# Kernel tuning notes

Measured on AMD Instinct MI355X. Metric: run time of the kernel, lower is better.

## Reference

```python
import jax, jax.numpy as jnp
import numpy as np

B, F, H = 32768, 128, 64  # batch, input_size, hidden width (n_layers=(64,64))


def setup_inputs() -> dict:
    key = jax.random.key(0)
    ks = jax.random.split(key, 8)
    s1 = 1.0  # fan_in=1 for first layer
    sH = 1.0 / np.sqrt(H)
    return {
        "x": jax.random.normal(ks[0], (B, F), dtype=jnp.float32),
        "w1": jax.random.uniform(ks[1], (F, H), jnp.float32, -s1, s1),
        "b1": jax.random.uniform(ks[2], (F, H), jnp.float32, -s1, s1),
        "w2": jax.random.uniform(ks[3], (F, H, H), jnp.float32, -sH, sH),
        "b2": jax.random.uniform(ks[4], (F, H), jnp.float32, -sH, sH),
        "w3": jax.random.uniform(ks[5], (F, H), jnp.float32, -sH, sH),
        "b3": jax.random.uniform(ks[6], (F,), jnp.float32, -sH, sH),
        "bias": jnp.zeros((1,), dtype=jnp.float32),
    }


def reference(x, w1, b1, w2, b2, w3, b3, bias):
    # Per-feature tiny MLP, batched over all F features at once.
    # Layer 1: Linear(1 -> H): h1[b,f,h] = x[b,f]*w1[f,h] + b1[f,h]
    h1 = jax.nn.relu(x[:, :, None] * w1[None] + b1[None])        # (B, F, H)
    # Layer 2: Linear(H -> H) per feature (grouped GEMM)
    h2 = jax.nn.relu(jnp.einsum("bfh,fhg->bfg", h1, w2) + b2[None])  # (B, F, H)
    # Output layer: Linear(H -> 1) per feature -> contribution (B, F)
    contrib = jnp.einsum("bfh,fh->bf", h2, w3) + b3[None]        # (B, F)
    logit = contrib.sum(axis=-1) + bias                          # (B,)
    p = jax.nn.sigmoid(logit)
    return jnp.stack([1.0 - p, p], axis=1)                       # (B, 2)
```

## Files before the change

kernel.cpp:

```cpp
#include <hip/hip_runtime.h>
#include <hip/hip_bf16.h>
#include <hip/hip_fp16.h>


#define B_SZ 32768
#define F_SZ 128
#define H_SZ 64

typedef _Float16 half8 __attribute__((ext_vector_type(8)));
typedef float floatx4 __attribute__((ext_vector_type(4)));

union U8 { half8 v; unsigned u[4]; };

__device__ __forceinline__ unsigned pkh(float lo, float hi) {
    __half2 h = __float22half2_rn(make_float2(lo, hi));
    return __builtin_bit_cast(unsigned, h);
}

__device__ __forceinline__ unsigned cpk(float lo, float hi) {
    return __builtin_bit_cast(unsigned, __builtin_amdgcn_cvt_pkrtz(lo, hi));
}

__device__ __forceinline__ unsigned relu2(unsigned a) {
    unsigned r;
    asm("v_pk_max_f16 %0, %1, %2" : "=v"(r) : "v"(a), "v"(0u));
    return r;
}

__device__ __forceinline__ float fdot2(unsigned a, unsigned b, float c) {
    float d;
    asm("v_dot2_f32_f16 %0, %1, %2, %3" : "=v"(d) : "v"(a), "v"(b), "v"(c));
    return d;
}

__device__ __forceinline__ __half2 bch2(unsigned u) {
    return __builtin_bit_cast(__half2, u);
}

__global__ __launch_bounds__(256, 3)
void nam_main(const float* __restrict__ x,
              const float* __restrict__ w1, const float* __restrict__ b1,
              const float* __restrict__ b2, const float* __restrict__ w3,
              const float* __restrict__ b3,
              const float* __restrict__ w2,
              float* __restrict__ part)
{
    __shared__ float partial[4][512];

    const int tid  = threadIdx.x;
    const int lane = tid & 63;
    const int wv   = tid >> 6;
    const int l15  = lane & 15;
    const int quad = lane >> 4;
    const int rg   = blockIdx.x & 63;
    const int gf   = blockIdx.x >> 6;
    const int f    = gf * 4 + wv;
    const int rb   = rg * 512;

    const float* w2f = w2 + (size_t)f * H_SZ * H_SZ;
    half8 wfrag[4][2];
    #pragma unroll
    for (int gt = 0; gt < 4; ++gt)
        #pragma unroll
        for (int ks = 0; ks < 2; ++ks) {
            const float* src = w2f + (ks * 32 + quad * 8) * H_SZ + gt * 16 + l15;
            U8 o;
            #pragma unroll
            for (int t = 0; t < 4; ++t)
                o.u[t] = pkh(src[(2 * t) * H_SZ], src[(2 * t + 1) * H_SZ]);
            wfrag[gt][ks] = o.v;
        }

    unsigned wk2[2][4], bk2[2][4];
    #pragma unroll
    for (int ks = 0; ks < 2; ++ks) {
        float wtmp[8], btmp[8];
        const float4* wq = (const float4*)(w1 + f * 64 + ks * 32 + quad * 8);
        const float4* bq = (const float4*)(b1 + f * 64 + ks * 32 + quad * 8);
        *(float4*)&wtmp[0] = wq[0]; *(float4*)&wtmp[4] = wq[1];
        *(float4*)&btmp[0] = bq[0]; *(float4*)&btmp[4] = bq[1];
        #pragma unroll
        for (int t = 0; t < 4; ++t) {
            wk2[ks][t] = pkh(wtmp[2 * t], wtmp[2 * t + 1]);
            bk2[ks][t] = pkh(btmp[2 * t], btmp[2 * t + 1]);
        }
    }

    floatx4 b2c[4];
    unsigned w3h[4][2];
    #pragma unroll
    for (int gt = 0; gt < 4; ++gt) {
        float4 bv  = *(const float4*)(b2 + f * 64 + gt * 16 + quad * 4);
        float4 wv3 = *(const float4*)(w3 + f * 64 + gt * 16 + quad * 4);
        b2c[gt] = floatx4{bv.x, bv.y, bv.z, bv.w};
        w3h[gt][0] = pkh(wv3.x, wv3.y);
        w3h[gt][1] = pkh(wv3.z, wv3.w);
    }
    const float b3f = b3[f];

    float xv = x[(size_t)(rb + lane) * F_SZ + f];

    #pragma unroll 1
    for (int c = 0; c < 8; ++c) {
        float xvn;
        if (c < 7)
            xvn = x[(size_t)(rb + (c + 1) * 64 + lane) * F_SZ + f];

        unsigned xpk = __builtin_bit_cast(unsigned, __float2half2_rn(xv));
        unsigned xf[4];
        #pragma unroll
        for (int bt = 0; bt < 4; ++bt)
            xf[bt] = (unsigned)__shfl((int)xpk, bt * 16 + l15, 64);

        half8 hfrag[4][2];
        #pragma unroll
        for (int ks = 0; ks < 2; ++ks)
            #pragma unroll
            for (int bt = 0; bt < 4; ++bt) {
                U8 o;
                #pragma unroll
                for (int t = 0; t < 4; ++t) {
                    __half2 h = __hfma2(bch2(xf[bt]), bch2(wk2[ks][t]), bch2(bk2[ks][t]));
                    o.u[t] = relu2(__builtin_bit_cast(unsigned, h));
                }
                hfrag[bt][ks] = o.v;
            }

        float ta[4] = {0.0f, 0.0f, 0.0f, 0.0f};
        float tb[4] = {0.0f, 0.0f, 0.0f, 0.0f};
        __builtin_amdgcn_s_setprio(1);
        #pragma unroll
        for (int gt = 0; gt < 4; ++gt)
            #pragma unroll
            for (int bt = 0; bt < 4; ++bt) {
                floatx4 acc = __builtin_amdgcn_mfma_f32_16x16x32_f16(
                    wfrag[gt][0], hfrag[bt][0], b2c[gt], 0, 0, 0);
                acc = __builtin_amdgcn_mfma_f32_16x16x32_f16(
                    wfrag[gt][1], hfrag[bt][1], acc, 0, 0, 0);
                unsigned p0 = relu2(cpk(acc[0], acc[1]));
                unsigned p1 = relu2(cpk(acc[2], acc[3]));
                ta[bt] = fdot2(p0, w3h[gt][0], ta[bt]);
                tb[bt] = fdot2(p1, w3h[gt][1], tb[bt]);
            }
        __builtin_amdgcn_s_setprio(0);

        float t[4];
        #pragma unroll
        for (int bt = 0; bt < 4; ++bt) {
            t[bt] = ta[bt] + tb[bt];
            t[bt] += __shfl_xor(t[bt], 16, 64);
            t[bt] += __shfl_xor(t[bt], 32, 64);
        }
        if (quad == 0) {
            #pragma unroll
            for (int bt = 0; bt < 4; ++bt)
                partial[wv][c * 64 + bt * 16 + l15] = t[bt] + b3f;
        }

        xv = xvn;
    }

    __syncthreads();

    #pragma unroll
    for (int k = 0; k < 2; ++k) {
        int row = k * 256 + tid;
        float p = partial[0][row] + partial[1][row]
                + partial[2][row] + partial[3][row];
        part[(size_t)gf * B_SZ + rb + row] = p;
    }
}

__global__ __launch_bounds__(256)
void nam_final(const float* __restrict__ part, const float* __restrict__ bias,
               float* __restrict__ out)
{
    int b = blockIdx.x * 256 + threadIdx.x;
    float s = bias[0];
    #pragma unroll
    for (int gf = 0; gf < 32; ++gf)
        s += part[(size_t)gf * B_SZ + b];
    float p = 1.0f / (1.0f + __expf(-s));
    ((float2*)out)[b] = make_float2(1.0f - p, p);
}

extern "C" void kernel_launch(void* const* d_in, const int* in_sizes, int n_in,
                              void* d_out, int out_size, void* d_ws, size_t ws_size,
                              hipStream_t stream)
{
    const float* x    = (const float*)d_in[0];
    const float* w1   = (const float*)d_in[1];
    const float* b1   = (const float*)d_in[2];
    const float* w2   = (const float*)d_in[3];
    const float* b2   = (const float*)d_in[4];
    const float* w3   = (const float*)d_in[5];
    const float* b3   = (const float*)d_in[6];
    const float* bias = (const float*)d_in[7];
    float* out = (float*)d_out;

    float* part = (float*)d_ws;

    nam_main<<<dim3(2048), dim3(256), 0, stream>>>(
        x, w1, b1, b2, w3, b3, w2, part);
    nam_final<<<dim3(B_SZ / 256), dim3(256), 0, stream>>>(part, bias, out);
}
```

Baseline: 115.9 us.

## Fuse final reduction into main kernel via atomics and last-block sigmoid

```diff
diff --git a/kernel.cpp b/kernel.cpp
--- a/kernel.cpp
+++ b/kernel.cpp
@@ -43,9 +43,13 @@
               const float* __restrict__ b2, const float* __restrict__ w3,
               const float* __restrict__ b3,
               const float* __restrict__ w2,
-              float* __restrict__ part)
+              const float* __restrict__ bias,
+              float* __restrict__ logitacc,
+              unsigned* __restrict__ cnt,
+              float* __restrict__ out)
 {
     __shared__ float partial[4][512];
+    __shared__ int lastFlag;
 
     const int tid  = threadIdx.x;
     const int lane = tid & 63;
@@ -167,21 +171,30 @@
         int row = k * 256 + tid;
         float p = partial[0][row] + partial[1][row]
                 + partial[2][row] + partial[3][row];
-        part[(size_t)gf * B_SZ + rb + row] = p;
-    }
-}
-
-__global__ __launch_bounds__(256)
-void nam_final(const float* __restrict__ part, const float* __restrict__ bias,
-               float* __restrict__ out)
-{
-    int b = blockIdx.x * 256 + threadIdx.x;
-    float s = bias[0];
-    #pragma unroll
-    for (int gf = 0; gf < 32; ++gf)
-        s += part[(size_t)gf * B_SZ + b];
-    float p = 1.0f / (1.0f + __expf(-s));
-    ((float2*)out)[b] = make_float2(1.0f - p, p);
+        atomicAdd(&logitacc[rb + row], p);
+    }
+
+    __threadfence();
+    __syncthreads();
+    if (tid == 0) {
+        unsigned old = __hip_atomic_fetch_add(&cnt[rg], 1u,
+                           __ATOMIC_ACQ_REL, __HIP_MEMORY_SCOPE_AGENT);
+        lastFlag = (old == 31u);
+    }
+    __syncthreads();
+
+    if (lastFlag) {
+        const float bsc = bias[0];
+        #pragma unroll
+        for (int k = 0; k < 2; ++k) {
+            int row = k * 256 + tid;
+            float s = __hip_atomic_load(&logitacc[rb + row],
+                          __ATOMIC_ACQUIRE, __HIP_MEMORY_SCOPE_AGENT);
+            s += bsc;
+            float p = 1.0f / (1.0f + __expf(-s));
+            ((float2*)out)[rb + row] = make_float2(1.0f - p, p);
+        }
+    }
 }
 
 extern "C" void kernel_launch(void* const* d_in, const int* in_sizes, int n_in,
@@ -198,9 +211,12 @@
     const float* bias = (const float*)d_in[7];
     float* out = (float*)d_out;
 
-    float* part = (float*)d_ws;
+    float* logitacc = (float*)d_ws;
+    unsigned* cnt   = (unsigned*)d_ws + B_SZ;
+
+    hipMemsetAsync(d_ws, 0, B_SZ * sizeof(float) + 64 * sizeof(unsigned),
+                   stream);
 
     nam_main<<<dim3(2048), dim3(256), 0, stream>>>(
-        x, w1, b1, b2, w3, b3, w2, part);
-    nam_final<<<dim3(B_SZ / 256), dim3(256), 0, stream>>>(part, bias, out);
-}
+        x, w1, b1, b2, w3, b3, w2, bias, logitacc, cnt, out);
+}
```

Result: slower. 289.6 us (+149.8%).
